# Kernel optimization log

Hardware: AMD Instinct MI355X
Metric: run time of the kernel (lower is better)

The kernel has to match this reference:

```python
import jax, jax.numpy as jnp
import numpy as np

N = 50000
IN_DIM = 512
HIDDEN = 64
OUT_DIM = 47
E1 = 800000
E2 = 1200000


def setup_inputs() -> dict:
    key = jax.random.key(0)
    ks = jax.random.split(key, 10)
    x = jax.random.normal(ks[0], (N, IN_DIM), dtype=jnp.float32)
    src1 = jax.random.randint(ks[1], (E1,), 0, N, dtype=jnp.int32)
    dst1 = jax.random.randint(ks[2], (E1,), 0, N, dtype=jnp.int32)
    w1 = jax.random.uniform(ks[3], (E1,), dtype=jnp.float32)
    src2 = jax.random.randint(ks[4], (E2,), 0, N, dtype=jnp.int32)
    dst2 = jax.random.randint(ks[5], (E2,), 0, N, dtype=jnp.int32)
    w2 = jax.random.uniform(ks[6], (E2,), dtype=jnp.float32)
    embed_w = jax.random.normal(ks[7], (IN_DIM, HIDDEN), dtype=jnp.float32) / np.sqrt(IN_DIM)
    embed_b = jnp.zeros((HIDDEN,), dtype=jnp.float32)
    total_dim = (2 ** 3 - 1) * HIDDEN  # k=2 -> 7*hidden
    cls_w = jax.random.normal(ks[8], (total_dim, OUT_DIM), dtype=jnp.float32) / np.sqrt(total_dim)
    cls_b = jnp.zeros((OUT_DIM,), dtype=jnp.float32)
    return {"x": x, "src1": src1, "dst1": dst1, "w1": w1,
            "src2": src2, "dst2": dst2, "w2": w2,
            "embed_w": embed_w, "embed_b": embed_b,
            "cls_w": cls_w, "cls_b": cls_b}


def _spmm(src, dst, w, h, n):
    # out[i] = sum_{e: dst[e]==i} w[e] * h[src[e]]  == sparse_adj @ h
    return jax.ops.segment_sum(w[:, None] * h[src], dst, num_segments=n)


def reference(x, src1, dst1, w1, src2, dst2, w2, embed_w, embed_b, cls_w, cls_b):
    k = 2
    # dropout is identity in eval mode
    h = jax.nn.relu(x @ embed_w + embed_b)  # [N, hidden]
    reps = [h]
    for _ in range(k):
        h1 = _spmm(src1, dst1, w1, h, N)  # strict 1-hop
        h2 = _spmm(src2, dst2, w2, h, N)  # strict 2-hop
        h = jax.nn.relu(jnp.concatenate([h1, h2], axis=1))
        reps.append(h)
    h_final = jnp.concatenate(reps, axis=1)  # [N, 7*hidden]
    return h_final @ cls_w + cls_b
```

## Files before the change

### kernel.cpp

```cpp
#include <hip/hip_runtime.h>

#define N_NODES 50000
#define IN_DIM 512
#define HIDDEN 64
#define OUT_DIM 47
#define HSTRIDE 448

#define NBINS 391
#define CAP1 3072
#define CAP2 4096
#define CHUNK 2048

typedef unsigned short u16;
typedef short v8s __attribute__((ext_vector_type(8)));
typedef float v4f __attribute__((ext_vector_type(4)));

union F4 { float4 v; float f[4]; };
union U4 { uint4 v; unsigned u[4]; };

static __device__ __forceinline__ u16 f2bf(float f) {
  unsigned u = __float_as_uint(f);
  u += 0x7fffu + ((u >> 16) & 1u);
  return (u16)(u >> 16);
}
static __device__ __forceinline__ float bf2f(u16 h) {
  return __uint_as_float(((unsigned)h) << 16);
}

__global__ __launch_bounds__(256) void conv_w(
    const float* __restrict__ embed_w, u16* __restrict__ weTh,
    u16* __restrict__ weTl, const float* __restrict__ cls_w,
    u16* __restrict__ wcTh, u16* __restrict__ wcTl) {
  int b = blockIdx.x;
  if (b < 16) {
    int tid = b * 256 + threadIdx.x;
    int col = tid >> 6;
    int k8 = (tid & 63) * 8;
#pragma unroll
    for (int j = 0; j < 8; j++) {
      float v = embed_w[(size_t)(k8 + j) * HIDDEN + col];
      u16 h = f2bf(v);
      weTh[(size_t)col * IN_DIM + k8 + j] = h;
      weTl[(size_t)col * IN_DIM + k8 + j] = f2bf(v - bf2f(h));
    }
  } else {
    int tid = (b - 16) * 256 + threadIdx.x;
    if (tid < 48 * 56) {
      int col = tid / 56;
      int k8 = (tid % 56) * 8;
#pragma unroll
      for (int j = 0; j < 8; j++) {
        float v = (col < OUT_DIM) ? cls_w[(size_t)(k8 + j) * OUT_DIM + col] : 0.f;
        u16 h = f2bf(v);
        wcTh[(size_t)col * HSTRIDE + k8 + j] = h;
        wcTl[(size_t)col * HSTRIDE + k8 + j] = f2bf(v - bf2f(h));
      }
    }
  }
}

__global__ __launch_bounds__(256) void bin_edges(
    const int* __restrict__ src1, const int* __restrict__ dst1,
    const float* __restrict__ w1, int E1, int c1,
    const int* __restrict__ src2, const int* __restrict__ dst2,
    const float* __restrict__ w2, int E2,
    int* __restrict__ binCursor, int2* __restrict__ stg1,
    int2* __restrict__ stg2) {
  __shared__ int hist[NBINS], sbase[NBINS], cur[NBINS], segrel[NBINS];
  __shared__ int wsum[4];
  __shared__ int2 buf[CHUNK];

  int q = blockIdx.x;
  const int *src, *dst;
  const float* w;
  int E, cap;
  int2* stg;
  int* bc;
  if (q < c1) {
    src = src1; dst = dst1; w = w1; E = E1; stg = stg1; bc = binCursor; cap = CAP1;
  } else {
    q -= c1;
    src = src2; dst = dst2; w = w2; E = E2; stg = stg2; bc = binCursor + NBINS; cap = CAP2;
  }
  int e0 = q * CHUNK;
  int n = E - e0;
  if (n > CHUNK) n = CHUNK;
  int t = threadIdx.x;

  for (int i = t; i < NBINS; i += 256) hist[i] = 0;
  __syncthreads();

  int2 pk[8];
#pragma unroll
  for (int j = 0; j < 8; j++) {
    int idx = t + j * 256;
    if (idx < n) {
      int d = dst[e0 + idx];
      int bin = d >> 7;
      pk[j] = make_int2(src[e0 + idx] | ((d & 127) << 16) | (bin << 23),
                        __float_as_int(w[e0 + idx]));
      atomicAdd(&hist[bin], 1);
    } else {
      pk[j].x = -1;
    }
  }
  __syncthreads();

  int a0 = 0, a1 = 0;
  if (t < 196) {
    a0 = hist[2 * t];
    if (2 * t + 1 < NBINS) a1 = hist[2 * t + 1];
  }
  int s = a0 + a1;
  int lane = t & 63, wid = t >> 6;
  int ps = s;
#pragma unroll
  for (int off = 1; off < 64; off <<= 1) {
    int v = __shfl_up(ps, off, 64);
    if (lane >= off) ps += v;
  }
  if (lane == 63) wsum[wid] = ps;
  __syncthreads();
  if (t == 0) {
    int c = 0;
#pragma unroll
    for (int i = 0; i < 4; i++) { int tmp = wsum[i]; wsum[i] = c; c += tmp; }
  }
  __syncthreads();
  int excl = ps - s + wsum[wid];
  if (t < 196) {
    sbase[2 * t] = excl;
    cur[2 * t] = excl;
    if (2 * t + 1 < NBINS) { sbase[2 * t + 1] = excl + a0; cur[2 * t + 1] = excl + a0; }
  }
  __syncthreads();

#pragma unroll
  for (int j = 0; j < 8; j++) {
    if (pk[j].x != -1) {
      int bin = (pk[j].x >> 23) & 0x1FF;
      int pos = atomicAdd(&cur[bin], 1);
      buf[pos] = pk[j];
    }
  }
  for (int i = t; i < NBINS; i += 256) {
    int h = hist[i];
    segrel[i] = h ? atomicAdd(&bc[i], h) : 0;
  }
  __syncthreads();

  for (int i = t; i < n; i += 256) {
    int2 e = buf[i];
    int bin = (e.x >> 23) & 0x1FF;
    int pos = segrel[bin] + (i - sbase[bin]);
    if (pos < cap)
      stg[(size_t)bin * cap + pos] = make_int2(e.x & 0x7FFFFF, e.y);
  }
}

__global__ __launch_bounds__(256) void embed_mfma(
    const float* __restrict__ x, const u16* __restrict__ wTh,
    const u16* __restrict__ wTl, const float* __restrict__ bias,
    u16* __restrict__ hcat) {
  int wave = threadIdx.x >> 6, lane = threadIdx.x & 63;
  int row0 = blockIdx.x * 64 + wave * 16;
  int m = lane & 15, kq = lane >> 4;
  int rowA = row0 + m;
  if (rowA >= N_NODES) rowA = N_NODES - 1;
  const float* xr = x + (size_t)rowA * IN_DIM;

  v4f acc[4];
#pragma unroll
  for (int nf = 0; nf < 4; nf++) acc[nf] = (v4f){0.f, 0.f, 0.f, 0.f};

#pragma unroll 4
  for (int k0 = 0; k0 < IN_DIM; k0 += 32) {
    int kk = k0 + kq * 8;
    F4 p, qv;
    p.v = *(const float4*)(xr + kk);
    qv.v = *(const float4*)(xr + kk + 4);
    v8s a;
#pragma unroll
    for (int j = 0; j < 4; j++) {
      a[j] = (short)f2bf(p.f[j]);
      a[4 + j] = (short)f2bf(qv.f[j]);
    }
#pragma unroll
    for (int nf = 0; nf < 4; nf++) {
      int col = nf * 16 + m;
      v8s bh = *(const v8s*)(wTh + (size_t)col * IN_DIM + kk);
      v8s bl = *(const v8s*)(wTl + (size_t)col * IN_DIM + kk);
      acc[nf] = __builtin_amdgcn_mfma_f32_16x16x32_bf16(a, bh, acc[nf], 0, 0, 0);
      acc[nf] = __builtin_amdgcn_mfma_f32_16x16x32_bf16(a, bl, acc[nf], 0, 0, 0);
    }
  }

#pragma unroll
  for (int nf = 0; nf < 4; nf++) {
    int col = nf * 16 + m;
    float bv = bias[col];
#pragma unroll
    for (int reg = 0; reg < 4; reg++) {
      int rowC = row0 + kq * 4 + reg;
      if (rowC < N_NODES) {
        float v = acc[nf][reg] + bv;
        hcat[(size_t)rowC * HSTRIDE + col] = f2bf(v > 0.f ? v : 0.f);
      }
    }
  }
}

__global__ __launch_bounds__(512) void binscan(const int* __restrict__ cnt,
                                               int* __restrict__ scanout) {
  const int* in = cnt + blockIdx.x * NBINS;
  int* out = scanout + blockIdx.x * NBINS;
  int tid = threadIdx.x, lane = tid & 63, wid = tid >> 6;
  __shared__ int wsum[8];
  int v0 = (tid < NBINS) ? in[tid] : 0;
  int v = v0;
#pragma unroll
  for (int off = 1; off < 64; off <<= 1) {
    int t = __shfl_up(v, off, 64);
    if (lane >= off) v += t;
  }
  if (lane == 63) wsum[wid] = v;
  __syncthreads();
  if (tid < 8) {
    int s = wsum[tid], sc = s;
#pragma unroll
    for (int off = 1; off < 8; off <<= 1) {
      int t = __shfl_up(sc, off, 8);
      if (tid >= off) sc += t;
    }
    wsum[tid] = sc - s;
  }
  __syncthreads();
  if (tid < NBINS) out[tid] = v - v0 + wsum[wid];
}

__global__ __launch_bounds__(256) void place(
    const int* __restrict__ binCursor, const int* __restrict__ binScan,
    const int2* __restrict__ stg1, int2* __restrict__ ew1,
    int* __restrict__ ep1, const int2* __restrict__ stg2,
    int2* __restrict__ ew2, int* __restrict__ ep2) {
  int pb = blockIdx.x;
  int lb = pb < NBINS ? pb : pb - NBINS;
  const int2* stg;
  int2* ew;
  int* ep;
  int cap;
  if (pb < NBINS) { stg = stg1; ew = ew1; ep = ep1; cap = CAP1; }
  else            { stg = stg2; ew = ew2; ep = ep2; cap = CAP2; }
  int cnt = binCursor[pb];
  if (cnt > cap) cnt = cap;
  int base = binScan[pb];
  const int2* seg = stg + (size_t)lb * cap;
  int node0 = lb << 7;
  int nnodes = N_NODES - node0;
  if (nnodes > 128) nnodes = 128;

  __shared__ int ncnt[128], noff[128], ncur[128];
  __shared__ int t0;
  if (threadIdx.x < 128) { ncnt[threadIdx.x] = 0; ncur[threadIdx.x] = 0; }
  __syncthreads();
  for (int t = threadIdx.x; t < cnt; t += 256)
    atomicAdd(&ncnt[(seg[t].x >> 16) & 127], 1);
  __syncthreads();
  int v0 = 0, v = 0;
  if (threadIdx.x < 128) {
    v0 = ncnt[threadIdx.x];
    v = v0;
    int lane = threadIdx.x & 63;
#pragma unroll
    for (int off = 1; off < 64; off <<= 1) {
      int t = __shfl_up(v, off, 64);
      if (lane >= off) v += t;
    }
    if (threadIdx.x == 63) t0 = v;
  }
  __syncthreads();
  if (threadIdx.x < 128) {
    int excl = v - v0 + (threadIdx.x >= 64 ? t0 : 0);
    noff[threadIdx.x] = excl;
    if (threadIdx.x < nnodes) ep[node0 + threadIdx.x] = base + excl + v0;
  }
  __syncthreads();
  for (int t = threadIdx.x; t < cnt; t += 256) {
    int2 pk = seg[t];
    int nl = (pk.x >> 16) & 127;
    int pos = base + noff[nl] + atomicAdd(&ncur[nl], 1);
    ew[pos] = make_int2(pk.x & 0xFFFF, pk.y);
  }
}

__device__ __forceinline__ void bf8_fma(const U4& r, float wt, float* a) {
#pragma unroll
  for (int i = 0; i < 4; i++) {
    a[2 * i]     += wt * __uint_as_float(r.u[i] << 16);
    a[2 * i + 1] += wt * __uint_as_float(r.u[i] & 0xffff0000u);
  }
}

template <int NT>
__global__ __launch_bounds__(256) void gather2(
    const int* __restrict__ ep1, const int2* __restrict__ ew1,
    const int* __restrict__ ep2, const int2* __restrict__ ew2,
    const u16* __restrict__ hin, u16* __restrict__ out1,
    u16* __restrict__ out2, int half_blocks) {
  int b = blockIdx.x;
  const int* ep;
  const int2* ew;
  u16* out;
  if (b < half_blocks) { ep = ep1; ew = ew1; out = out1; }
  else { b -= half_blocks; ep = ep2; ew = ew2; out = out2; }

  int tid = b * 256 + threadIdx.x;
  int node = tid / NT;
  if (node >= N_NODES) return;
  int col0 = (tid % NT) * 8;
  int s = node ? ep[node - 1] : 0;
  int e = ep[node];

  float a0[8], a1[8];
#pragma unroll
  for (int i = 0; i < 8; i++) { a0[i] = 0.f; a1[i] = 0.f; }

  int j = s;
  for (; j + 4 <= e; j += 4) {
    int2 p0 = ew[j], p1 = ew[j + 1], p2 = ew[j + 2], p3 = ew[j + 3];
    U4 r0, r1, r2, r3;
    r0.v = *(const uint4*)(hin + (size_t)p0.x * HSTRIDE + col0);
    r1.v = *(const uint4*)(hin + (size_t)p1.x * HSTRIDE + col0);
    r2.v = *(const uint4*)(hin + (size_t)p2.x * HSTRIDE + col0);
    r3.v = *(const uint4*)(hin + (size_t)p3.x * HSTRIDE + col0);
    bf8_fma(r0, __int_as_float(p0.y), a0);
    bf8_fma(r1, __int_as_float(p1.y), a1);
    bf8_fma(r2, __int_as_float(p2.y), a0);
    bf8_fma(r3, __int_as_float(p3.y), a1);
  }
  for (; j < e; j++) {
    int2 p = ew[j];
    U4 r;
    r.v = *(const uint4*)(hin + (size_t)p.x * HSTRIDE + col0);
    bf8_fma(r, __int_as_float(p.y), a0);
  }

  U4 o;
#pragma unroll
  for (int i = 0; i < 4; i++) {
    float lo = a0[2 * i] + a1[2 * i];
    float hi = a0[2 * i + 1] + a1[2 * i + 1];
    lo = lo > 0.f ? lo : 0.f;
    hi = hi > 0.f ? hi : 0.f;
    o.u[i] = ((unsigned)f2bf(hi) << 16) | (unsigned)f2bf(lo);
  }
  *(uint4*)(out + (size_t)node * HSTRIDE + col0) = o.v;
}

__global__ __launch_bounds__(256) void final_mfma(
    const u16* __restrict__ hcat, const u16* __restrict__ wTh,
    const u16* __restrict__ wTl, const float* __restrict__ bias,
    float* __restrict__ out) {
  int wave = threadIdx.x >> 6, lane = threadIdx.x & 63;
  int row0 = blockIdx.x * 64 + wave * 16;
  int m = lane & 15, kq = lane >> 4;
  int rowA = row0 + m;
  if (rowA >= N_NODES) rowA = N_NODES - 1;
  const u16* hr = hcat + (size_t)rowA * HSTRIDE;

  v4f acc[3];
#pragma unroll
  for (int nf = 0; nf < 3; nf++) acc[nf] = (v4f){0.f, 0.f, 0.f, 0.f};

#pragma unroll 2
  for (int k0 = 0; k0 < HSTRIDE; k0 += 32) {
    int kk = k0 + kq * 8;
    v8s a = *(const v8s*)(hr + kk);
#pragma unroll
    for (int nf = 0; nf < 3; nf++) {
      int col = nf * 16 + m;
      v8s bh = *(const v8s*)(wTh + (size_t)col * HSTRIDE + kk);
      v8s bl = *(const v8s*)(wTl + (size_t)col * HSTRIDE + kk);
      acc[nf] = __builtin_amdgcn_mfma_f32_16x16x32_bf16(a, bh, acc[nf], 0, 0, 0);
      acc[nf] = __builtin_amdgcn_mfma_f32_16x16x32_bf16(a, bl, acc[nf], 0, 0, 0);
    }
  }

#pragma unroll
  for (int nf = 0; nf < 3; nf++) {
    int col = nf * 16 + m;
    if (col < OUT_DIM) {
      float bv = bias[col];
#pragma unroll
      for (int reg = 0; reg < 4; reg++) {
        int rowC = row0 + kq * 4 + reg;
        if (rowC < N_NODES)
          out[(size_t)rowC * OUT_DIM + col] = acc[nf][reg] + bv;
      }
    }
  }
}

extern "C" void kernel_launch(void* const* d_in, const int* in_sizes, int n_in,
                              void* d_out, int out_size, void* d_ws,
                              size_t ws_size, hipStream_t stream) {
  const float* x       = (const float*)d_in[0];
  const int*   src1    = (const int*)d_in[1];
  const int*   dst1    = (const int*)d_in[2];
  const float* w1      = (const float*)d_in[3];
  const int*   src2    = (const int*)d_in[4];
  const int*   dst2    = (const int*)d_in[5];
  const float* w2      = (const float*)d_in[6];
  const float* embed_w = (const float*)d_in[7];
  const float* embed_b = (const float*)d_in[8];
  const float* cls_w   = (const float*)d_in[9];
  const float* cls_b   = (const float*)d_in[10];
  int E1 = in_sizes[1];
  int E2 = in_sizes[4];

  float* ws = (float*)d_ws;
  size_t off = 0;
  u16* hcat = (u16*)(ws + off); off += (size_t)N_NODES * HSTRIDE / 2;
  int2* ew1 = (int2*)(ws + off); off += (size_t)2 * E1;
  int2* ew2 = (int2*)(ws + off); off += (size_t)2 * E2;
  int* ep1 = (int*)(ws + off); off += N_NODES;
  int* ep2 = (int*)(ws + off); off += N_NODES;
  int2* stg1 = (int2*)(ws + off); off += (size_t)2 * NBINS * CAP1;
  int2* stg2 = (int2*)(ws + off); off += (size_t)2 * NBINS * CAP2;
  int* binCursor = (int*)(ws + off); off += 2 * NBINS;
  int* binScan = (int*)(ws + off); off += 2 * NBINS;
  u16* weTh = (u16*)(ws + off); off += 16384;
  u16* weTl = (u16*)(ws + off); off += 16384;
  u16* wcTh = (u16*)(ws + off); off += 10752;
  u16* wcTl = (u16*)(ws + off); off += 10752;

  int c1 = (E1 + CHUNK - 1) / CHUNK;
  int c2 = (E2 + CHUNK - 1) / CHUNK;

  hipMemsetAsync(binCursor, 0, 2 * NBINS * sizeof(int), stream);
  conv_w<<<27, 256, 0, stream>>>(embed_w, weTh, weTl, cls_w, wcTh, wcTl);
  bin_edges<<<c1 + c2, 256, 0, stream>>>(
      src1, dst1, w1, E1, c1, src2, dst2, w2, E2, binCursor, stg1, stg2);
  embed_mfma<<<782, 256, 0, stream>>>(x, weTh, weTl, embed_b, hcat);
  binscan<<<2, 512, 0, stream>>>(binCursor, binScan);
  place<<<2 * NBINS, 256, 0, stream>>>(binCursor, binScan,
                                       stg1, ew1, ep1, stg2, ew2, ep2);
  gather2<8><<<3126, 256, 0, stream>>>(ep1, ew1, ep2, ew2, hcat,
                                       hcat + 64, hcat + 128, 1563);
  gather2<16><<<6250, 256, 0, stream>>>(ep1, ew1, ep2, ew2, hcat + 64,
                                        hcat + 192, hcat + 320, 3125);
  final_mfma<<<782, 256, 0, stream>>>(hcat, wcTh, wcTl, cls_b, (float*)d_out);
}
```

Measured before the change: 281.0 us.

## Fuse weight conversion into edge binning and split embed GEMM across waves by column

```diff
diff --git a/kernel.cpp b/kernel.cpp
--- a/kernel.cpp
+++ b/kernel.cpp
@@ -27,39 +27,10 @@
   return __uint_as_float(((unsigned)h) << 16);
 }
 
-__global__ __launch_bounds__(256) void conv_w(
+__global__ __launch_bounds__(256) void prep(
     const float* __restrict__ embed_w, u16* __restrict__ weTh,
     u16* __restrict__ weTl, const float* __restrict__ cls_w,
-    u16* __restrict__ wcTh, u16* __restrict__ wcTl) {
-  int b = blockIdx.x;
-  if (b < 16) {
-    int tid = b * 256 + threadIdx.x;
-    int col = tid >> 6;
-    int k8 = (tid & 63) * 8;
-#pragma unroll
-    for (int j = 0; j < 8; j++) {
-      float v = embed_w[(size_t)(k8 + j) * HIDDEN + col];
-      u16 h = f2bf(v);
-      weTh[(size_t)col * IN_DIM + k8 + j] = h;
-      weTl[(size_t)col * IN_DIM + k8 + j] = f2bf(v - bf2f(h));
-    }
-  } else {
-    int tid = (b - 16) * 256 + threadIdx.x;
-    if (tid < 48 * 56) {
-      int col = tid / 56;
-      int k8 = (tid % 56) * 8;
-#pragma unroll
-      for (int j = 0; j < 8; j++) {
-        float v = (col < OUT_DIM) ? cls_w[(size_t)(k8 + j) * OUT_DIM + col] : 0.f;
-        u16 h = f2bf(v);
-        wcTh[(size_t)col * HSTRIDE + k8 + j] = h;
-        wcTl[(size_t)col * HSTRIDE + k8 + j] = f2bf(v - bf2f(h));
-      }
-    }
-  }
-}
-
-__global__ __launch_bounds__(256) void bin_edges(
+    u16* __restrict__ wcTh, u16* __restrict__ wcTl,
     const int* __restrict__ src1, const int* __restrict__ dst1,
     const float* __restrict__ w1, int E1, int c1,
     const int* __restrict__ src2, const int* __restrict__ dst2,
@@ -70,7 +41,37 @@
   __shared__ int wsum[4];
   __shared__ int2 buf[CHUNK];
 
-  int q = blockIdx.x;
+  int b = blockIdx.x;
+  if (b < 16) {
+    int tid = b * 256 + threadIdx.x;
+    int col = tid >> 6;
+    int k8 = (tid & 63) * 8;
+#pragma unroll
+    for (int j = 0; j < 8; j++) {
+      float v = embed_w[(size_t)(k8 + j) * HIDDEN + col];
+      u16 h = f2bf(v);
+      weTh[(size_t)col * IN_DIM + k8 + j] = h;
+      weTl[(size_t)col * IN_DIM + k8 + j] = f2bf(v - bf2f(h));
+    }
+    return;
+  }
+  if (b < 27) {
+    int tid = (b - 16) * 256 + threadIdx.x;
+    if (tid < 48 * 56) {
+      int col = tid / 56;
+      int k8 = (tid % 56) * 8;
+#pragma unroll
+      for (int j = 0; j < 8; j++) {
+        float v = (col < OUT_DIM) ? cls_w[(size_t)(k8 + j) * OUT_DIM + col] : 0.f;
+        u16 h = f2bf(v);
+        wcTh[(size_t)col * HSTRIDE + k8 + j] = h;
+        wcTl[(size_t)col * HSTRIDE + k8 + j] = f2bf(v - bf2f(h));
+      }
+    }
+    return;
+  }
+
+  int q = b - 27;
   const int *src, *dst;
   const float* w;
   int E, cap;
@@ -163,17 +164,18 @@
     const u16* __restrict__ wTl, const float* __restrict__ bias,
     u16* __restrict__ hcat) {
   int wave = threadIdx.x >> 6, lane = threadIdx.x & 63;
-  int row0 = blockIdx.x * 64 + wave * 16;
+  int row0 = blockIdx.x * 16;
   int m = lane & 15, kq = lane >> 4;
   int rowA = row0 + m;
   if (rowA >= N_NODES) rowA = N_NODES - 1;
   const float* xr = x + (size_t)rowA * IN_DIM;
-
-  v4f acc[4];
-#pragma unroll
-  for (int nf = 0; nf < 4; nf++) acc[nf] = (v4f){0.f, 0.f, 0.f, 0.f};
-
-#pragma unroll 4
+  int col = wave * 16 + m;
+  const u16* bhp = wTh + (size_t)col * IN_DIM;
+  const u16* blp = wTl + (size_t)col * IN_DIM;
+
+  v4f acc = (v4f){0.f, 0.f, 0.f, 0.f};
+
+#pragma unroll 8
   for (int k0 = 0; k0 < IN_DIM; k0 += 32) {
     int kk = k0 + kq * 8;
     F4 p, qv;
@@ -185,27 +187,19 @@
       a[j] = (short)f2bf(p.f[j]);
       a[4 + j] = (short)f2bf(qv.f[j]);
     }
-#pragma unroll
-    for (int nf = 0; nf < 4; nf++) {
-      int col = nf * 16 + m;
-      v8s bh = *(const v8s*)(wTh + (size_t)col * IN_DIM + kk);
-      v8s bl = *(const v8s*)(wTl + (size_t)col * IN_DIM + kk);
-      acc[nf] = __builtin_amdgcn_mfma_f32_16x16x32_bf16(a, bh, acc[nf], 0, 0, 0);
-      acc[nf] = __builtin_amdgcn_mfma_f32_16x16x32_bf16(a, bl, acc[nf], 0, 0, 0);
-    }
-  }
-
-#pragma unroll
-  for (int nf = 0; nf < 4; nf++) {
-    int col = nf * 16 + m;
-    float bv = bias[col];
-#pragma unroll
-    for (int reg = 0; reg < 4; reg++) {
-      int rowC = row0 + kq * 4 + reg;
-      if (rowC < N_NODES) {
-        float v = acc[nf][reg] + bv;
-        hcat[(size_t)rowC * HSTRIDE + col] = f2bf(v > 0.f ? v : 0.f);
-      }
+    v8s bh = *(const v8s*)(bhp + kk);
+    v8s bl = *(const v8s*)(blp + kk);
+    acc = __builtin_amdgcn_mfma_f32_16x16x32_bf16(a, bh, acc, 0, 0, 0);
+    acc = __builtin_amdgcn_mfma_f32_16x16x32_bf16(a, bl, acc, 0, 0, 0);
+  }
+
+  float bv = bias[col];
+#pragma unroll
+  for (int reg = 0; reg < 4; reg++) {
+    int rowC = row0 + kq * 4 + reg;
+    if (rowC < N_NODES) {
+      float v = acc[reg] + bv;
+      hcat[(size_t)rowC * HSTRIDE + col] = f2bf(v > 0.f ? v : 0.f);
     }
   }
 }
@@ -438,10 +432,11 @@
   int c2 = (E2 + CHUNK - 1) / CHUNK;
 
   hipMemsetAsync(binCursor, 0, 2 * NBINS * sizeof(int), stream);
-  conv_w<<<27, 256, 0, stream>>>(embed_w, weTh, weTl, cls_w, wcTh, wcTl);
-  bin_edges<<<c1 + c2, 256, 0, stream>>>(
-      src1, dst1, w1, E1, c1, src2, dst2, w2, E2, binCursor, stg1, stg2);
-  embed_mfma<<<782, 256, 0, stream>>>(x, weTh, weTl, embed_b, hcat);
+  prep<<<27 + c1 + c2, 256, 0, stream>>>(
+      embed_w, weTh, weTl, cls_w, wcTh, wcTl,
+      src1, dst1, w1, E1, c1, src2, dst2, w2, E2,
+      binCursor, stg1, stg2);
+  embed_mfma<<<3125, 256, 0, stream>>>(x, weTh, weTl, embed_b, hcat);
   binscan<<<2, 512, 0, stream>>>(binCursor, binScan);
   place<<<2 * NBINS, 256, 0, stream>>>(binCursor, binScan,
                                        stg1, ew1, ep1, stg2, ew2, ep2);
```

Result: slower. 294.9 us (+4.9%).

## Merge x bf16 conversion into binning launch and fuse embed GEMM with place

Applied to the files above, without the earlier changes.

```diff
diff --git a/kernel.cpp b/kernel.cpp
--- a/kernel.cpp
+++ b/kernel.cpp
@@ -10,6 +10,7 @@
 #define CAP1 3072
 #define CAP2 4096
 #define CHUNK 2048
+#define XB 1024
 
 typedef unsigned short u16;
 typedef short v8s __attribute__((ext_vector_type(8)));
@@ -27,39 +28,11 @@
   return __uint_as_float(((unsigned)h) << 16);
 }
 
-__global__ __launch_bounds__(256) void conv_w(
+__global__ __launch_bounds__(256) void prep(
     const float* __restrict__ embed_w, u16* __restrict__ weTh,
     u16* __restrict__ weTl, const float* __restrict__ cls_w,
-    u16* __restrict__ wcTh, u16* __restrict__ wcTl) {
-  int b = blockIdx.x;
-  if (b < 16) {
-    int tid = b * 256 + threadIdx.x;
-    int col = tid >> 6;
-    int k8 = (tid & 63) * 8;
-#pragma unroll
-    for (int j = 0; j < 8; j++) {
-      float v = embed_w[(size_t)(k8 + j) * HIDDEN + col];
-      u16 h = f2bf(v);
-      weTh[(size_t)col * IN_DIM + k8 + j] = h;
-      weTl[(size_t)col * IN_DIM + k8 + j] = f2bf(v - bf2f(h));
-    }
-  } else {
-    int tid = (b - 16) * 256 + threadIdx.x;
-    if (tid < 48 * 56) {
-      int col = tid / 56;
-      int k8 = (tid % 56) * 8;
-#pragma unroll
-      for (int j = 0; j < 8; j++) {
-        float v = (col < OUT_DIM) ? cls_w[(size_t)(k8 + j) * OUT_DIM + col] : 0.f;
-        u16 h = f2bf(v);
-        wcTh[(size_t)col * HSTRIDE + k8 + j] = h;
-        wcTl[(size_t)col * HSTRIDE + k8 + j] = f2bf(v - bf2f(h));
-      }
-    }
-  }
-}
-
-__global__ __launch_bounds__(256) void bin_edges(
+    u16* __restrict__ wcTh, u16* __restrict__ wcTl,
+    const float* __restrict__ x, u16* __restrict__ x_bf,
     const int* __restrict__ src1, const int* __restrict__ dst1,
     const float* __restrict__ w1, int E1, int c1,
     const int* __restrict__ src2, const int* __restrict__ dst2,
@@ -70,7 +43,53 @@
   __shared__ int wsum[4];
   __shared__ int2 buf[CHUNK];
 
-  int q = blockIdx.x;
+  int b = blockIdx.x;
+  if (b < 16) {
+    int tid = b * 256 + threadIdx.x;
+    int col = tid >> 6;
+    int k8 = (tid & 63) * 8;
+#pragma unroll
+    for (int j = 0; j < 8; j++) {
+      float v = embed_w[(size_t)(k8 + j) * HIDDEN + col];
+      u16 h = f2bf(v);
+      weTh[(size_t)col * IN_DIM + k8 + j] = h;
+      weTl[(size_t)col * IN_DIM + k8 + j] = f2bf(v - bf2f(h));
+    }
+    return;
+  }
+  if (b < 27) {
+    int tid = (b - 16) * 256 + threadIdx.x;
+    if (tid < 48 * 56) {
+      int col = tid / 56;
+      int k8 = (tid % 56) * 8;
+#pragma unroll
+      for (int j = 0; j < 8; j++) {
+        float v = (col < OUT_DIM) ? cls_w[(size_t)(k8 + j) * OUT_DIM + col] : 0.f;
+        u16 h = f2bf(v);
+        wcTh[(size_t)col * HSTRIDE + k8 + j] = h;
+        wcTl[(size_t)col * HSTRIDE + k8 + j] = f2bf(v - bf2f(h));
+      }
+    }
+    return;
+  }
+  if (b < 27 + XB) {
+    const float4* x4 = (const float4*)x;
+    uint2* o2 = (uint2*)x_bf;
+    int i0 = (b - 27) * 256 + threadIdx.x;
+    int stride = XB * 256;
+    int tot = N_NODES * IN_DIM / 4;
+    for (int i = i0; i < tot; i += stride) {
+      F4 v;
+      v.v = x4[i];
+      uint2 o;
+      o.x = (unsigned)f2bf(v.f[0]) | ((unsigned)f2bf(v.f[1]) << 16);
+      o.y = (unsigned)f2bf(v.f[2]) | ((unsigned)f2bf(v.f[3]) << 16);
+      o2[i] = o;
+    }
+    return;
+  }
+
+  int q = b - 27 - XB;
   const int *src, *dst;
   const float* w;
   int E, cap;
@@ -158,58 +177,6 @@
   }
 }
 
-__global__ __launch_bounds__(256) void embed_mfma(
-    const float* __restrict__ x, const u16* __restrict__ wTh,
-    const u16* __restrict__ wTl, const float* __restrict__ bias,
-    u16* __restrict__ hcat) {
-  int wave = threadIdx.x >> 6, lane = threadIdx.x & 63;
-  int row0 = blockIdx.x * 64 + wave * 16;
-  int m = lane & 15, kq = lane >> 4;
-  int rowA = row0 + m;
-  if (rowA >= N_NODES) rowA = N_NODES - 1;
-  const float* xr = x + (size_t)rowA * IN_DIM;
-
-  v4f acc[4];
-#pragma unroll
-  for (int nf = 0; nf < 4; nf++) acc[nf] = (v4f){0.f, 0.f, 0.f, 0.f};
-
-#pragma unroll 4
-  for (int k0 = 0; k0 < IN_DIM; k0 += 32) {
-    int kk = k0 + kq * 8;
-    F4 p, qv;
-    p.v = *(const float4*)(xr + kk);
-    qv.v = *(const float4*)(xr + kk + 4);
-    v8s a;
-#pragma unroll
-    for (int j = 0; j < 4; j++) {
-      a[j] = (short)f2bf(p.f[j]);
-      a[4 + j] = (short)f2bf(qv.f[j]);
-    }
-#pragma unroll
-    for (int nf = 0; nf < 4; nf++) {
-      int col = nf * 16 + m;
-      v8s bh = *(const v8s*)(wTh + (size_t)col * IN_DIM + kk);
-      v8s bl = *(const v8s*)(wTl + (size_t)col * IN_DIM + kk);
-      acc[nf] = __builtin_amdgcn_mfma_f32_16x16x32_bf16(a, bh, acc[nf], 0, 0, 0);
-      acc[nf] = __builtin_amdgcn_mfma_f32_16x16x32_bf16(a, bl, acc[nf], 0, 0, 0);
-    }
-  }
-
-#pragma unroll
-  for (int nf = 0; nf < 4; nf++) {
-    int col = nf * 16 + m;
-    float bv = bias[col];
-#pragma unroll
-    for (int reg = 0; reg < 4; reg++) {
-      int rowC = row0 + kq * 4 + reg;
-      if (rowC < N_NODES) {
-        float v = acc[nf][reg] + bv;
-        hcat[(size_t)rowC * HSTRIDE + col] = f2bf(v > 0.f ? v : 0.f);
-      }
-    }
-  }
-}
-
 __global__ __launch_bounds__(512) void binscan(const int* __restrict__ cnt,
                                                int* __restrict__ scanout) {
   const int* in = cnt + blockIdx.x * NBINS;
@@ -238,12 +205,58 @@
   if (tid < NBINS) out[tid] = v - v0 + wsum[wid];
 }
 
-__global__ __launch_bounds__(256) void place(
-    const int* __restrict__ binCursor, const int* __restrict__ binScan,
-    const int2* __restrict__ stg1, int2* __restrict__ ew1,
-    int* __restrict__ ep1, const int2* __restrict__ stg2,
-    int2* __restrict__ ew2, int* __restrict__ ep2) {
-  int pb = blockIdx.x;
+__global__ __launch_bounds__(256) void embed_place(
+    const u16* __restrict__ x_bf, const u16* __restrict__ wTh,
+    const u16* __restrict__ wTl, const float* __restrict__ bias,
+    u16* __restrict__ hcat, const int* __restrict__ binCursor,
+    const int* __restrict__ binScan, const int2* __restrict__ stg1,
+    int2* __restrict__ ew1, int* __restrict__ ep1,
+    const int2* __restrict__ stg2, int2* __restrict__ ew2,
+    int* __restrict__ ep2) {
+  int b = blockIdx.x;
+  if (b < 782) {
+    int wave = threadIdx.x >> 6, lane = threadIdx.x & 63;
+    int row0 = b * 64 + wave * 16;
+    int m = lane & 15, kq = lane >> 4;
+    int rowA = row0 + m;
+    if (rowA >= N_NODES) rowA = N_NODES - 1;
+    const u16* xr = x_bf + (size_t)rowA * IN_DIM;
+
+    v4f acc[4];
+#pragma unroll
+    for (int nf = 0; nf < 4; nf++) acc[nf] = (v4f){0.f, 0.f, 0.f, 0.f};
+
+#pragma unroll 4
+    for (int k0 = 0; k0 < IN_DIM; k0 += 32) {
+      int kk = k0 + kq * 8;
+      v8s a = *(const v8s*)(xr + kk);
+#pragma unroll
+      for (int nf = 0; nf < 4; nf++) {
+        int col = nf * 16 + m;
+        v8s bh = *(const v8s*)(wTh + (size_t)col * IN_DIM + kk);
+        v8s bl = *(const v8s*)(wTl + (size_t)col * IN_DIM + kk);
+        acc[nf] = __builtin_amdgcn_mfma_f32_16x16x32_bf16(a, bh, acc[nf], 0, 0, 0);
+        acc[nf] = __builtin_amdgcn_mfma_f32_16x16x32_bf16(a, bl, acc[nf], 0, 0, 0);
+      }
+    }
+
+#pragma unroll
+    for (int nf = 0; nf < 4; nf++) {
+      int col = nf * 16 + m;
+      float bv = bias[col];
+#pragma unroll
+      for (int reg = 0; reg < 4; reg++) {
+        int rowC = row0 + kq * 4 + reg;
+        if (rowC < N_NODES) {
+          float v = acc[nf][reg] + bv;
+          hcat[(size_t)rowC * HSTRIDE + col] = f2bf(v > 0.f ? v : 0.f);
+        }
+      }
+    }
+    return;
+  }
+
+  int pb = b - 782;
   int lb = pb < NBINS ? pb : pb - NBINS;
   const int2* stg;
   int2* ew;
@@ -433,18 +446,20 @@
   u16* weTl = (u16*)(ws + off); off += 16384;
   u16* wcTh = (u16*)(ws + off); off += 10752;
   u16* wcTl = (u16*)(ws + off); off += 10752;
+  u16* x_bf = (u16*)(ws + off); off += (size_t)N_NODES * IN_DIM / 2;
 
   int c1 = (E1 + CHUNK - 1) / CHUNK;
   int c2 = (E2 + CHUNK - 1) / CHUNK;
 
   hipMemsetAsync(binCursor, 0, 2 * NBINS * sizeof(int), stream);
-  conv_w<<<27, 256, 0, stream>>>(embed_w, weTh, weTl, cls_w, wcTh, wcTl);
-  bin_edges<<<c1 + c2, 256, 0, stream>>>(
-      src1, dst1, w1, E1, c1, src2, dst2, w2, E2, binCursor, stg1, stg2);
-  embed_mfma<<<782, 256, 0, stream>>>(x, weTh, weTl, embed_b, hcat);
+  prep<<<27 + XB + c1 + c2, 256, 0, stream>>>(
+      embed_w, weTh, weTl, cls_w, wcTh, wcTl, x, x_bf,
+      src1, dst1, w1, E1, c1, src2, dst2, w2, E2,
+      binCursor, stg1, stg2);
   binscan<<<2, 512, 0, stream>>>(binCursor, binScan);
-  place<<<2 * NBINS, 256, 0, stream>>>(binCursor, binScan,
-                                       stg1, ew1, ep1, stg2, ew2, ep2);
+  embed_place<<<782 + 2 * NBINS, 256, 0, stream>>>(
+      x_bf, weTh, weTl, embed_b, hcat, binCursor, binScan,
+      stg1, ew1, ep1, stg2, ew2, ep2);
   gather2<8><<<3126, 256, 0, stream>>>(ep1, ew1, ep2, ew2, hcat,
                                        hcat + 64, hcat + 128, 1563);
   gather2<16><<<6250, 256, 0, stream>>>(ep1, ew1, ep2, ew2, hcat + 64,
```

After: 271.5 us. 3.4% less time.
